# Performance work log

Hardware: AMD Instinct MI355X
Metric: run time of the kernel (lower is better)

The kernel has to match this reference:

```python
import jax, jax.numpy as jnp
import numpy as np

B, S, D = 2, 2048, 512
H = 8
G = 4
LAMBDA_INIT = 0.2  # 0.8 - 0.6*exp(-0.3*(layer_idx-1)) with layer_idx=1
EPS = 1e-5


def setup_inputs() -> dict:
    key = jax.random.key(0)
    ks = jax.random.split(key, 16)
    n = jax.random.normal
    return {
        "x": n(ks[0], (B, S, D), jnp.float32),
        "K1_w": n(ks[1], (D, D), jnp.float32) * 0.02,
        "K1_b": n(ks[2], (D,), jnp.float32) * 0.02,
        "Q1_w": n(ks[3], (D, D), jnp.float32) * 0.02,
        "K2_w": n(ks[4], (D, D), jnp.float32) * 0.02,
        "K2_b": n(ks[5], (D,), jnp.float32) * 0.02,
        "Q2_w": n(ks[6], (D, D), jnp.float32) * 0.02,
        "V_w": n(ks[7], (D, D), jnp.float32) * 0.02,
        "lambda_q1": n(ks[8], (H, 1), jnp.float32),
        "lambda_k1": n(ks[9], (H, 1), jnp.float32),
        "lambda_q2": n(ks[10], (H, 1), jnp.float32),
        "lambda_k2": n(ks[11], (H, 1), jnp.float32),
        "gn_w": jnp.ones((D,), jnp.float32),
        "gn_b": jnp.zeros((D,), jnp.float32),
        "out_w": n(ks[12], (D, D), jnp.float32) * 0.02,
        "out_b": n(ks[13], (D,), jnp.float32) * 0.02,
    }


def reference(x, K1_w, K1_b, Q1_w, K2_w, K2_b, Q2_w, V_w,
              lambda_q1, lambda_k1, lambda_q2, lambda_k2,
              gn_w, gn_b, out_w, out_b):
    b, s, d = x.shape
    hd = d // H

    def heads(t):  # (b,s,d) -> (b,H,s,hd)
        return t.reshape(b, s, H, hd).transpose(0, 2, 1, 3)

    q1 = heads(x @ Q1_w.T)
    k1 = heads(x @ K1_w.T + K1_b)
    q2 = heads(x @ Q2_w.T)
    k2 = heads(x @ K2_w.T + K2_b)
    v = heads(x @ V_w.T)

    scale = hd ** 0.5
    a1 = jax.nn.softmax(jnp.einsum('bhqd,bhkd->bhqk', q1, k1) / scale, axis=-1)
    a2 = jax.nn.softmax(jnp.einsum('bhqd,bhkd->bhqk', q2, k2) / scale, axis=-1)

    lam = (jnp.exp(lambda_q1 * lambda_k1)
           - jnp.exp(lambda_q2 * lambda_k2) + LAMBDA_INIT)  # (H,1)
    attn = a1 - lam.reshape(1, H, 1, 1) * a2

    o = jnp.einsum('bhqk,bhkd->bhqd', attn, v)
    o = o.transpose(0, 2, 1, 3).reshape(b, s, d)

    # GroupNorm over channels: input (b, d, s), groups G normalize over (d/G, s)
    xc = o.transpose(0, 2, 1).reshape(b, G, d // G, s)
    mu = xc.mean(axis=(2, 3), keepdims=True)
    var = xc.var(axis=(2, 3), keepdims=True)
    xn = ((xc - mu) * jax.lax.rsqrt(var + EPS)).reshape(b, d, s)
    xn = xn * gn_w[None, :, None] + gn_b[None, :, None]

    y = xn.transpose(0, 2, 1) @ out_w.T + out_b
    return y
```

## Files before the change

kernel.cpp:

```cpp
#include <hip/hip_runtime.h>
#include <hip/hip_bf16.h>

typedef __bf16 bf16;
typedef __attribute__((ext_vector_type(8))) __bf16 bf16x8;
typedef __attribute__((ext_vector_type(4))) float f32x4;

#define MFMA16(a, b, c) __builtin_amdgcn_mfma_f32_16x16x32_bf16((a), (b), (c), 0, 0, 0)

static constexpr float EPS = 1e-5f;
static constexpr float LAMBDA_INIT = 0.2f;
static constexpr float LOG2E = 1.44269504088896340736f;

__device__ __forceinline__ bf16x8 cvt8(const float* p) {
    const f32x4 a = *(const f32x4*)p;
    const f32x4 b = *(const f32x4*)(p + 4);
    bf16x8 r;
    r[0] = (bf16)a[0]; r[1] = (bf16)a[1]; r[2] = (bf16)a[2]; r[3] = (bf16)a[3];
    r[4] = (bf16)b[0]; r[5] = (bf16)b[1]; r[6] = (bf16)b[2]; r[7] = (bf16)b[3];
    return r;
}

__device__ __forceinline__ void gload_lds16(const void* g, void* l) {
    __builtin_amdgcn_global_load_lds(
        (const __attribute__((address_space(1))) unsigned int*)g,
        (__attribute__((address_space(3))) unsigned int*)l,
        16, 0, 0);
}

__global__ __launch_bounds__(256) void prep_kernel(
    const float* __restrict__ x,
    const float* __restrict__ q1w, const float* __restrict__ k1w,
    const float* __restrict__ q2w, const float* __restrict__ k2w,
    const float* __restrict__ vw,
    const float* __restrict__ ow, const float* __restrict__ gnw,
    const float* __restrict__ gnb,
    bf16* __restrict__ xb, bf16* __restrict__ wb,
    bf16* __restrict__ owg, float* __restrict__ S0, float* __restrict__ stats)
{
    const int tid = threadIdx.x;
    if (blockIdx.x < 1664) {
        const size_t base = ((size_t)blockIdx.x * 256 + tid) * 8;
        if (base < 2097152) {
            *(bf16x8*)(xb + base) = cvt8(x + base);
        } else {
            const size_t wbase = base - 2097152;
            const int wsel = (int)(wbase >> 18);
            const size_t off = wbase & 262143;
            const float* W = (wsel == 0) ? q1w : (wsel == 1) ? k1w :
                             (wsel == 2) ? q2w : (wsel == 3) ? k2w : vw;
            *(bf16x8*)(wb + wbase) = cvt8(W + off);
        }
        return;
    }

    __shared__ float red[4];
    const int pb = blockIdx.x - 1664;
    if (pb == 0 && tid < 16) stats[tid] = 0.f;

    const int n0 = pb * 16;
    const int c0 = tid, c1 = tid + 256;
    const float gw0 = gnw[c0], gw1 = gnw[c1];
    const float gb0 = gnb[c0], gb1 = gnb[c1];

    for (int n = 0; n < 16; ++n) {
        const size_t rowb = (size_t)(n0 + n) * 512;
        const float w0 = ow[rowb + c0];
        const float w1 = ow[rowb + c1];
        owg[rowb + c0] = (bf16)(w0 * gw0);
        owg[rowb + c1] = (bf16)(w1 * gw1);
        float s = gb0 * w0 + gb1 * w1;
#pragma unroll
        for (int off = 1; off < 64; off <<= 1) s += __shfl_xor(s, off, 64);
        if ((tid & 63) == 0) red[tid >> 6] = s;
        __syncthreads();
        if (tid == 0) S0[n0 + n] = red[0] + red[1] + red[2] + red[3];
        __syncthreads();
    }
}

__global__ __launch_bounds__(256) void proj_kernel(
    const bf16* __restrict__ xb, const bf16* __restrict__ wb,
    const float* __restrict__ k1b, const float* __restrict__ k2b,
    bf16* __restrict__ q1o, bf16* __restrict__ k1o,
    bf16* __restrict__ q2o, bf16* __restrict__ k2o,
    bf16* __restrict__ vto)
{
    __shared__ __align__(16) bf16 As[2][128 * 32];
    __shared__ __align__(16) bf16 Bs[2][128 * 32];

    const int tid = threadIdx.x;
    const int wave = tid >> 6, lane = tid & 63;
    const int l15 = lane & 15, quad = lane >> 4;
    const int wm = wave >> 1, wn = wave & 1;

    const int mb = blockIdx.x / 20;
    const int nb = blockIdx.x % 20;
    const int wsel = nb >> 2;
    const int nrow0 = (nb & 3) * 128;

    const int srow = lane >> 2;
    const int scol = (lane & 3) * 8;
    const bf16* ag = xb + (size_t)(mb * 128 + srow) * 512 + scol;
    const bf16* bg = wb + (size_t)(wsel * 512 + nrow0 + srow) * 512 + scol;

    f32x4 acc[4][4];
#pragma unroll
    for (int i = 0; i < 4; ++i)
#pragma unroll
        for (int j = 0; j < 4; ++j)
            acc[i][j] = (f32x4){0.f, 0.f, 0.f, 0.f};

#pragma unroll
    for (int c = 0; c < 2; ++c) {
        const int chunk = wave * 2 + c;
        gload_lds16(ag + (size_t)(chunk * 16) * 512, As[0] + chunk * 512);
        gload_lds16(bg + (size_t)(chunk * 16) * 512, Bs[0] + chunk * 512);
    }
    __syncthreads();

    for (int s = 0; s < 16; ++s) {
        const int cur = s & 1;
        if (s < 15) {
            const int k0n = (s + 1) * 32;
#pragma unroll
            for (int c = 0; c < 2; ++c) {
                const int chunk = wave * 2 + c;
                gload_lds16(ag + (size_t)(chunk * 16) * 512 + k0n, As[cur ^ 1] + chunk * 512);
                gload_lds16(bg + (size_t)(chunk * 16) * 512 + k0n, Bs[cur ^ 1] + chunk * 512);
            }
        }

        const bf16* Ac = As[cur];
        const bf16* Bc = Bs[cur];
        bf16x8 af[4], bfr[4];
#pragma unroll
        for (int i = 0; i < 4; ++i)
            af[i] = *(const bf16x8*)(Ac + (wm * 64 + i * 16 + l15) * 32 + quad * 8);
#pragma unroll
        for (int j = 0; j < 4; ++j)
            bfr[j] = *(const bf16x8*)(Bc + (wn * 64 + j * 16 + l15) * 32 + quad * 8);

#pragma unroll
        for (int i = 0; i < 4; ++i)
#pragma unroll
            for (int j = 0; j < 4; ++j)
                acc[i][j] = MFMA16(af[i], bfr[j], acc[i][j]);

        __syncthreads();
    }

    const float scale = (wsel == 0 || wsel == 2) ? 0.125f * LOG2E : 1.0f;
#pragma unroll
    for (int j = 0; j < 4; ++j) {
        const int ncol = nrow0 + wn * 64 + j * 16 + l15;
        float bias = 0.f;
        if (wsel == 1) bias = k1b[ncol];
        if (wsel == 3) bias = k2b[ncol];
        const int h = ncol >> 6, hd = ncol & 63;
        const int xh = (hd >> 1) & 3;
#pragma unroll
        for (int i = 0; i < 4; ++i) {
#pragma unroll
            for (int r = 0; r < 4; ++r) {
                const int m = mb * 128 + wm * 64 + i * 16 + quad * 4 + r;
                const int bidx = m >> 11, s = m & 2047;
                const float v = acc[i][j][r] * scale + bias;
                if (wsel == 4) {
                    const int s5 = s & 31;
                    const int q = (s5 >> 2) & 3;
                    const int jj = (s5 & 3) + ((s5 >> 4) << 2);
                    const int p = ((q ^ xh) << 3) | jj;
                    const int sp = (s & ~31) | p;
                    vto[((size_t)(bidx * 8 + h) * 64 + hd) * 2048 + sp] = (bf16)v;
                } else {
                    bf16* dst = (wsel == 0) ? q1o : (wsel == 1) ? k1o :
                                (wsel == 2) ? q2o : k2o;
                    dst[((size_t)(bidx * 8 + h) * 2048 + s) * 64 + hd] = (bf16)v;
                }
            }
        }
    }
}

__global__ __launch_bounds__(512, 4) void attn_kernel(
    const bf16* __restrict__ q1, const bf16* __restrict__ k1,
    const bf16* __restrict__ q2, const bf16* __restrict__ k2,
    const bf16* __restrict__ vt,
    const float* __restrict__ lq1, const float* __restrict__ lk1,
    const float* __restrict__ lq2, const float* __restrict__ lk2,
    bf16* __restrict__ o, float* __restrict__ stats)
{
    __shared__ __align__(16) bf16 smem[2][12288];
    __shared__ float lbuf[8][2][16];
    __shared__ float sred[8][2];

    const int tid = threadIdx.x;
    const int wave = tid >> 6;
    const int lane = tid & 63;
    const int l15 = lane & 15, quad = lane >> 4;
    const int qtile = wave & 3;
    const int kg = wave >> 2;

    const int rid = (blockIdx.x & 7) * 64 + (blockIdx.x >> 3);
    const int bh = rid >> 5;
    const int qt = rid & 31;
    const int b = bh >> 3, h = bh & 7;

    const bf16* k1t = k1 + (size_t)bh * 2048 * 64;
    const bf16* k2t = k2 + (size_t)bh * 2048 * 64;
    const bf16* vtt = vt + (size_t)bh * 64 * 2048;

    const int qrow = qt * 64 + qtile * 16 + l15;
    const bf16* q1p = q1 + ((size_t)bh * 2048 + qrow) * 64 + quad * 8;
    const bf16* q2p = q2 + ((size_t)bh * 2048 + qrow) * 64 + quad * 8;
    const bf16x8 q1f0 = *(const bf16x8*)(q1p);
    const bf16x8 q1f1 = *(const bf16x8*)(q1p + 32);
    const bf16x8 q2f0 = *(const bf16x8*)(q2p);
    const bf16x8 q2f1 = *(const bf16x8*)(q2p + 32);

    const int sw = wave & 3;
    const int skey0 = (wave < 4) ? 0 : 1024;
    const size_t ksrc0 = (size_t)(skey0 + sw * 8 + (lane >> 3)) * 64
                       + 8 * ((lane & 7) ^ (lane >> 3));
    const size_t vsrc0 = (size_t)(sw * 16 + (lane >> 2)) * 2048 + skey0 + (lane & 3) * 8;

    const int koffa = 8 * (quad ^ (l15 & 7));
    const int koffb = 8 * ((quad + 4) ^ (l15 & 7));
    const int vsw = 8 * (quad ^ ((l15 >> 1) & 3));

    f32x4 O1[4], O2[4];
    float l1 = 0.f, l2 = 0.f;
#pragma unroll
    for (int t = 0; t < 4; ++t) {
        O1[t] = (f32x4){0.f, 0.f, 0.f, 0.f};
        O2[t] = (f32x4){0.f, 0.f, 0.f, 0.f};
    }

    gload_lds16(k1t + ksrc0, smem[0] + wave * 512);
    gload_lds16(k2t + ksrc0, smem[0] + 4096 + wave * 512);
    gload_lds16(vtt + vsrc0, smem[0] + 8192 + wave * 512);
    __syncthreads();

    for (int it = 0; it < 32; ++it) {
        const int cur = it & 1;
        const bf16* sb = smem[cur];

        if (it < 31) {
            bf16* nb_ = smem[cur ^ 1];
            const size_t koff = ksrc0 + (size_t)(it + 1) * 32 * 64;
            gload_lds16(k1t + koff, nb_ + wave * 512);
            gload_lds16(k2t + koff, nb_ + 4096 + wave * 512);
            gload_lds16(vtt + vsrc0 + (it + 1) * 32, nb_ + 8192 + wave * 512);
        }

        const bf16* k1r = sb + kg * 2048;
        const bf16* k2r = sb + 4096 + kg * 2048;
        const bf16* vr  = sb + 8192 + kg * 2048;

        const bf16x8 k1t0a = *(const bf16x8*)(k1r + l15 * 64 + koffa);
        const bf16x8 k1t0b = *(const bf16x8*)(k1r + l15 * 64 + koffb);
        const bf16x8 k1t1a = *(const bf16x8*)(k1r + (16 + l15) * 64 + koffa);
        const bf16x8 k1t1b = *(const bf16x8*)(k1r + (16 + l15) * 64 + koffb);
        const bf16x8 k2t0a = *(const bf16x8*)(k2r + l15 * 64 + koffa);
        const bf16x8 k2t0b = *(const bf16x8*)(k2r + l15 * 64 + koffb);
        const bf16x8 k2t1a = *(const bf16x8*)(k2r + (16 + l15) * 64 + koffa);
        const bf16x8 k2t1b = *(const bf16x8*)(k2r + (16 + l15) * 64 + koffb);
        const bf16x8 v0 = *(const bf16x8*)(vr + l15 * 32 + vsw);
        const bf16x8 v1 = *(const bf16x8*)(vr + (16 + l15) * 32 + vsw);
        const bf16x8 v2 = *(const bf16x8*)(vr + (32 + l15) * 32 + vsw);
        const bf16x8 v3 = *(const bf16x8*)(vr + (48 + l15) * 32 + vsw);

        f32x4 z = (f32x4){0.f, 0.f, 0.f, 0.f};
        f32x4 s1t0 = MFMA16(k1t0a, q1f0, z);  s1t0 = MFMA16(k1t0b, q1f1, s1t0);
        f32x4 s1t1 = MFMA16(k1t1a, q1f0, z);  s1t1 = MFMA16(k1t1b, q1f1, s1t1);
        f32x4 s2t0 = MFMA16(k2t0a, q2f0, z);  s2t0 = MFMA16(k2t0b, q2f1, s2t0);
        f32x4 s2t1 = MFMA16(k2t1a, q2f0, z);  s2t1 = MFMA16(k2t1b, q2f1, s2t1);

        bf16x8 b1, b2;
#pragma unroll
        for (int r = 0; r < 4; ++r) {
            float e;
            e = __builtin_amdgcn_exp2f(s1t0[r]); l1 += e; b1[r]     = (bf16)e;
            e = __builtin_amdgcn_exp2f(s1t1[r]); l1 += e; b1[4 + r] = (bf16)e;
            e = __builtin_amdgcn_exp2f(s2t0[r]); l2 += e; b2[r]     = (bf16)e;
            e = __builtin_amdgcn_exp2f(s2t1[r]); l2 += e; b2[4 + r] = (bf16)e;
        }

        O1[0] = MFMA16(v0, b1, O1[0]);
        O1[1] = MFMA16(v1, b1, O1[1]);
        O1[2] = MFMA16(v2, b1, O1[2]);
        O1[3] = MFMA16(v3, b1, O1[3]);
        O2[0] = MFMA16(v0, b2, O2[0]);
        O2[1] = MFMA16(v1, b2, O2[1]);
        O2[2] = MFMA16(v2, b2, O2[2]);
        O2[3] = MFMA16(v3, b2, O2[3]);

        __syncthreads();
    }

    l1 += __shfl_xor(l1, 16, 64);  l1 += __shfl_xor(l1, 32, 64);
    l2 += __shfl_xor(l2, 16, 64);  l2 += __shfl_xor(l2, 32, 64);
    if (lane < 16) {
        lbuf[wave][0][lane] = l1;
        lbuf[wave][1][lane] = l2;
    }
    __syncthreads();

    f32x4* rb = (f32x4*)smem;
    if (wave == 4 || wave == 5) {
        f32x4* dst = rb + (wave - 4) * 512;
#pragma unroll
        for (int t = 0; t < 4; ++t) {
            dst[t * 64 + lane]       = O1[t];
            dst[(4 + t) * 64 + lane] = O2[t];
        }
    }
    __syncthreads();
    if (wave == 0 || wave == 1) {
        const f32x4* src = rb + wave * 512;
#pragma unroll
        for (int t = 0; t < 4; ++t) {
            O1[t] += src[t * 64 + lane];
            O2[t] += src[(4 + t) * 64 + lane];
        }
    }
    __syncthreads();
    if (wave == 6 || wave == 7) {
        f32x4* dst = rb + (wave - 6) * 512;
#pragma unroll
        for (int t = 0; t < 4; ++t) {
            dst[t * 64 + lane]       = O1[t];
            dst[(4 + t) * 64 + lane] = O2[t];
        }
    }
    __syncthreads();
    if (wave == 2 || wave == 3) {
        const f32x4* src = rb + (wave - 2) * 512;
#pragma unroll
        for (int t = 0; t < 4; ++t) {
            O1[t] += src[t * 64 + lane];
            O2[t] += src[(4 + t) * 64 + lane];
        }
    }

    float ssum = 0.f, ssq = 0.f;
    if (wave < 4) {
        const float L1 = l1 + lbuf[wave + 4][0][l15];
        const float L2 = l2 + lbuf[wave + 4][1][l15];
        const float lam = __expf(lq1[h] * lk1[h]) - __expf(lq2[h] * lk2[h]) + LAMBDA_INIT;
        const float inv1 = 1.f / L1;
        const float inv2 = lam / L2;
        const size_t row = (size_t)(b * 2048 + qt * 64 + wave * 16 + l15) * 512 + h * 64;
#pragma unroll
        for (int t = 0; t < 4; ++t) {
#pragma unroll
            for (int r = 0; r < 4; ++r) {
                const float val = O1[t][r] * inv1 - O2[t][r] * inv2;
                ssum += val;
                ssq += val * val;
                o[row + t * 16 + quad * 4 + r] = (bf16)val;
            }
        }
    }
#pragma unroll
    for (int off = 1; off < 64; off <<= 1) {
        ssum += __shfl_xor(ssum, off, 64);
        ssq += __shfl_xor(ssq, off, 64);
    }
    if (lane == 0) { sred[wave][0] = ssum; sred[wave][1] = ssq; }
    __syncthreads();
    if (tid == 0) {
        float s0 = 0.f, s1 = 0.f;
        for (int w = 0; w < 8; ++w) { s0 += sred[w][0]; s1 += sred[w][1]; }
        const int bg = b * 4 + (h >> 1);
        atomicAdd(&stats[bg * 2], s0);
        atomicAdd(&stats[bg * 2 + 1], s1);
    }
}

__global__ __launch_bounds__(256) void out_gemm_kernel(
    const bf16* __restrict__ o, const bf16* __restrict__ owg,
    const float* __restrict__ S0, const float* __restrict__ stats,
    const float* __restrict__ ob, float* __restrict__ y)
{
    __shared__ __align__(16) bf16 As[2][64 * 32];
    __shared__ __align__(16) bf16 Bs[2][64 * 32];

    const int tid = threadIdx.x;
    const int wave = tid >> 6, lane = tid & 63;
    const int l15 = lane & 15, quad = lane >> 4;

    const int mb = blockIdx.x >> 3;
    const int nb = blockIdx.x & 7;
    const int b = mb >> 5;

    const float N = 128.f * 2048.f;
    float mu[4], rs[4];
#pragma unroll
    for (int g = 0; g < 4; ++g) {
        const float m = stats[(b * 4 + g) * 2] / N;
        const float var = stats[(b * 4 + g) * 2 + 1] / N - m * m;
        mu[g] = m;
        rs[g] = rsqrtf(var + EPS);
    }

    const int srow = wave * 16 + (lane >> 2);
    const int scol = (lane & 3) * 8;
    const bf16* ag = o + (size_t)(mb * 64 + srow) * 512 + scol;
    const bf16* bg = owg + (size_t)(nb * 64 + srow) * 512 + scol;

    f32x4 acc[4], tot[4];
#pragma unroll
    for (int i = 0; i < 4; ++i) {
        acc[i] = (f32x4){0.f, 0.f, 0.f, 0.f};
        tot[i] = (f32x4){0.f, 0.f, 0.f, 0.f};
    }
    float s1g[4];
    float s1p = 0.f;
#pragma unroll
    for (int g = 0; g < 4; ++g) s1g[g] = 0.f;

    gload_lds16(ag, As[0] + wave * 512);
    gload_lds16(bg, Bs[0] + wave * 512);
    __syncthreads();

    for (int kk = 0; kk < 16; ++kk) {
        const int cur = kk & 1;
        if (kk < 15) {
            gload_lds16(ag + (kk + 1) * 32, As[cur ^ 1] + wave * 512);
            gload_lds16(bg + (kk + 1) * 32, Bs[cur ^ 1] + wave * 512);
        }

        bf16x8 af[4];
#pragma unroll
        for (int i = 0; i < 4; ++i)
            af[i] = *(const bf16x8*)(As[cur] + (i * 16 + l15) * 32 + quad * 8);
        const bf16x8 bf = *(const bf16x8*)(Bs[cur] + (wave * 16 + l15) * 32 + quad * 8);

#pragma unroll
        for (int i = 0; i < 4; ++i)
            acc[i] = MFMA16(af[i], bf, acc[i]);

#pragma unroll
        for (int j = 0; j < 8; ++j) s1p += (float)bf[j];

        __syncthreads();

        if ((kk & 3) == 3) {
            const int g = kk >> 2;
#pragma unroll
            for (int i = 0; i < 4; ++i) {
#pragma unroll
                for (int r = 0; r < 4; ++r) tot[i][r] += rs[g] * acc[i][r];
                acc[i] = (f32x4){0.f, 0.f, 0.f, 0.f};
            }
            float sg = s1p + __shfl_xor(s1p, 16, 64);
            sg += __shfl_xor(sg, 32, 64);
            s1g[g] = sg;
            s1p = 0.f;
        }
    }

    const int ncol = nb * 64 + wave * 16 + l15;
    float bias = S0[ncol] + ob[ncol];
#pragma unroll
    for (int g = 0; g < 4; ++g) bias -= mu[g] * rs[g] * s1g[g];

#pragma unroll
    for (int i = 0; i < 4; ++i) {
#pragma unroll
        for (int r = 0; r < 4; ++r) {
            const int m = mb * 64 + i * 16 + quad * 4 + r;
            y[(size_t)m * 512 + ncol] = tot[i][r] + bias;
        }
    }
}

extern "C" void kernel_launch(void* const* d_in, const int* in_sizes, int n_in,
                              void* d_out, int out_size, void* d_ws, size_t ws_size,
                              hipStream_t stream)
{
    const float* x   = (const float*)d_in[0];
    const float* K1w = (const float*)d_in[1];
    const float* K1b = (const float*)d_in[2];
    const float* Q1w = (const float*)d_in[3];
    const float* K2w = (const float*)d_in[4];
    const float* K2b = (const float*)d_in[5];
    const float* Q2w = (const float*)d_in[6];
    const float* Vw  = (const float*)d_in[7];
    const float* lq1 = (const float*)d_in[8];
    const float* lk1 = (const float*)d_in[9];
    const float* lq2 = (const float*)d_in[10];
    const float* lk2 = (const float*)d_in[11];
    const float* gnw = (const float*)d_in[12];
    const float* gnb = (const float*)d_in[13];
    const float* Ow  = (const float*)d_in[14];
    const float* Ob  = (const float*)d_in[15];

    const size_t SZ = (size_t)2 * 8 * 2048 * 64;
    bf16* q1 = (bf16*)d_ws;
    bf16* k1 = q1 + SZ;
    bf16* q2 = k1 + SZ;
    bf16* k2 = q2 + SZ;
    bf16* vt = k2 + SZ;
    bf16* o  = vt + SZ;
    bf16* xb = o;
    bf16* wb = o + SZ;
    bf16* owg = wb + (size_t)2560 * 512;
    float* S0 = (float*)(owg + 512 * 512);
    float* stats = S0 + 512;

    prep_kernel<<<1696, 256, 0, stream>>>(x, Q1w, K1w, Q2w, K2w, Vw,
                                          Ow, gnw, gnb, xb, wb, owg, S0, stats);
    proj_kernel<<<640, 256, 0, stream>>>(xb, wb, K1b, K2b,
                                         q1, k1, q2, k2, vt);
    attn_kernel<<<512, 512, 0, stream>>>(q1, k1, q2, k2, vt,
                                         lq1, lk1, lq2, lk2, o, stats);
    out_gemm_kernel<<<512, 256, 0, stream>>>(o, owg, S0, stats, Ob,
                                             (float*)d_out);
}
```

Baseline: 181.7 us.

## Widen GEMM K-tiles to 64 with swizzled LDS and halve attention waves

The projection and output GEMMs now stage K-tiles of 64 instead of 32 through an XOR-swizzled LDS layout. This halves the number of barrier-separated iterations and is meant to cut bank conflicts. The attention kernel drops from 8 to 4 waves per block, with each wave handling two 16-row query tiles so every K/V fragment read from LDS is reused twice. It also adds s_setprio around the MFMA bursts and simplifies the cross-wave reduction. In exchange, register pressure rises and fewer waves are resident to hide latency.

```diff
diff --git a/kernel.cpp b/kernel.cpp
--- a/kernel.cpp
+++ b/kernel.cpp
@@ -85,8 +85,8 @@
     bf16* __restrict__ q2o, bf16* __restrict__ k2o,
     bf16* __restrict__ vto)
 {
-    __shared__ __align__(16) bf16 As[2][128 * 32];
-    __shared__ __align__(16) bf16 Bs[2][128 * 32];
+    __shared__ __align__(16) bf16 As[2][128 * 64];
+    __shared__ __align__(16) bf16 Bs[2][128 * 64];
 
     const int tid = threadIdx.x;
     const int wave = tid >> 6, lane = tid & 63;
@@ -98,8 +98,8 @@
     const int wsel = nb >> 2;
     const int nrow0 = (nb & 3) * 128;
 
-    const int srow = lane >> 2;
-    const int scol = (lane & 3) * 8;
+    const int srow = lane >> 3;
+    const int scol = 8 * ((lane & 7) ^ srow);
     const bf16* ag = xb + (size_t)(mb * 128 + srow) * 512 + scol;
     const bf16* bg = wb + (size_t)(wsel * 512 + nrow0 + srow) * 512 + scol;
 
@@ -110,41 +110,48 @@
         for (int j = 0; j < 4; ++j)
             acc[i][j] = (f32x4){0.f, 0.f, 0.f, 0.f};
 
-#pragma unroll
-    for (int c = 0; c < 2; ++c) {
-        const int chunk = wave * 2 + c;
-        gload_lds16(ag + (size_t)(chunk * 16) * 512, As[0] + chunk * 512);
-        gload_lds16(bg + (size_t)(chunk * 16) * 512, Bs[0] + chunk * 512);
-    }
+#define STAGE_PROJ(buf, s) do {                                                \
+    const int k0_ = (s) * 64;                                                  \
+    _Pragma("unroll")                                                          \
+    for (int c_ = 0; c_ < 4; ++c_) {                                           \
+        const int chunk_ = wave * 4 + c_;                                      \
+        gload_lds16(ag + (size_t)(chunk_ * 8) * 512 + k0_, As[buf] + chunk_ * 512); \
+        gload_lds16(bg + (size_t)(chunk_ * 8) * 512 + k0_, Bs[buf] + chunk_ * 512); \
+    }                                                                          \
+} while (0)
+
+    STAGE_PROJ(0, 0);
     __syncthreads();
 
-    for (int s = 0; s < 16; ++s) {
+    const int ka = 8 * (quad ^ (l15 & 7));
+
+    for (int s = 0; s < 8; ++s) {
         const int cur = s & 1;
-        if (s < 15) {
-            const int k0n = (s + 1) * 32;
-#pragma unroll
-            for (int c = 0; c < 2; ++c) {
-                const int chunk = wave * 2 + c;
-                gload_lds16(ag + (size_t)(chunk * 16) * 512 + k0n, As[cur ^ 1] + chunk * 512);
-                gload_lds16(bg + (size_t)(chunk * 16) * 512 + k0n, Bs[cur ^ 1] + chunk * 512);
-            }
-        }
+        if (s < 7) STAGE_PROJ(cur ^ 1, s + 1);
 
         const bf16* Ac = As[cur];
         const bf16* Bc = Bs[cur];
-        bf16x8 af[4], bfr[4];
+        bf16x8 al[4], ah[4], bl[4], bh_[4];
+#pragma unroll
+        for (int i = 0; i < 4; ++i) {
+            const bf16* p = Ac + (wm * 64 + i * 16 + l15) * 64;
+            al[i] = *(const bf16x8*)(p + ka);
+            ah[i] = *(const bf16x8*)(p + (ka ^ 32));
+        }
+#pragma unroll
+        for (int j = 0; j < 4; ++j) {
+            const bf16* p = Bc + (wn * 64 + j * 16 + l15) * 64;
+            bl[j]  = *(const bf16x8*)(p + ka);
+            bh_[j] = *(const bf16x8*)(p + (ka ^ 32));
+        }
+
 #pragma unroll
         for (int i = 0; i < 4; ++i)
-            af[i] = *(const bf16x8*)(Ac + (wm * 64 + i * 16 + l15) * 32 + quad * 8);
-#pragma unroll
-        for (int j = 0; j < 4; ++j)
-            bfr[j] = *(const bf16x8*)(Bc + (wn * 64 + j * 16 + l15) * 32 + quad * 8);
-
-#pragma unroll
-        for (int i = 0; i < 4; ++i)
-#pragma unroll
-            for (int j = 0; j < 4; ++j)
-                acc[i][j] = MFMA16(af[i], bfr[j], acc[i][j]);
+#pragma unroll
+            for (int j = 0; j < 4; ++j) {
+                acc[i][j] = MFMA16(al[i], bl[j], acc[i][j]);
+                acc[i][j] = MFMA16(ah[i], bh_[j], acc[i][j]);
+            }
 
         __syncthreads();
     }
@@ -182,7 +189,7 @@
     }
 }
 
-__global__ __launch_bounds__(512, 4) void attn_kernel(
+__global__ __launch_bounds__(256, 2) void attn_kernel(
     const bf16* __restrict__ q1, const bf16* __restrict__ k1,
     const bf16* __restrict__ q2, const bf16* __restrict__ k2,
     const bf16* __restrict__ vt,
@@ -191,15 +198,15 @@
     bf16* __restrict__ o, float* __restrict__ stats)
 {
     __shared__ __align__(16) bf16 smem[2][12288];
-    __shared__ float lbuf[8][2][16];
-    __shared__ float sred[8][2];
+    __shared__ float lbuf[4][4][16];
+    __shared__ float sred[2][2];
 
     const int tid = threadIdx.x;
     const int wave = tid >> 6;
     const int lane = tid & 63;
     const int l15 = lane & 15, quad = lane >> 4;
-    const int qtile = wave & 3;
-    const int kg = wave >> 2;
+    const int qp = wave & 1;
+    const int kg = wave >> 1;
 
     const int rid = (blockIdx.x & 7) * 64 + (blockIdx.x >> 3);
     const int bh = rid >> 5;
@@ -210,48 +217,57 @@
     const bf16* k2t = k2 + (size_t)bh * 2048 * 64;
     const bf16* vtt = vt + (size_t)bh * 64 * 2048;
 
-    const int qrow = qt * 64 + qtile * 16 + l15;
+    const int qrow = qt * 64 + qp * 32 + l15;
     const bf16* q1p = q1 + ((size_t)bh * 2048 + qrow) * 64 + quad * 8;
     const bf16* q2p = q2 + ((size_t)bh * 2048 + qrow) * 64 + quad * 8;
-    const bf16x8 q1f0 = *(const bf16x8*)(q1p);
-    const bf16x8 q1f1 = *(const bf16x8*)(q1p + 32);
-    const bf16x8 q2f0 = *(const bf16x8*)(q2p);
-    const bf16x8 q2f1 = *(const bf16x8*)(q2p + 32);
-
-    const int sw = wave & 3;
-    const int skey0 = (wave < 4) ? 0 : 1024;
-    const size_t ksrc0 = (size_t)(skey0 + sw * 8 + (lane >> 3)) * 64
-                       + 8 * ((lane & 7) ^ (lane >> 3));
-    const size_t vsrc0 = (size_t)(sw * 16 + (lane >> 2)) * 2048 + skey0 + (lane & 3) * 8;
+    const bf16x8 q1A0 = *(const bf16x8*)(q1p);
+    const bf16x8 q1A1 = *(const bf16x8*)(q1p + 32);
+    const bf16x8 q1B0 = *(const bf16x8*)(q1p + 16 * 64);
+    const bf16x8 q1B1 = *(const bf16x8*)(q1p + 16 * 64 + 32);
+    const bf16x8 q2A0 = *(const bf16x8*)(q2p);
+    const bf16x8 q2A1 = *(const bf16x8*)(q2p + 32);
+    const bf16x8 q2B0 = *(const bf16x8*)(q2p + 16 * 64);
+    const bf16x8 q2B1 = *(const bf16x8*)(q2p + 16 * 64 + 32);
+
+    const int krow = lane >> 3;
+    const int kcol = 8 * ((lane & 7) ^ krow);
+    const int ko0 = (wave * 8 + krow) * 64 + kcol;
+    const int ko1 = (1024 + wave * 8 + krow) * 64 + kcol;
+    const int vrow = lane >> 2;
+    const int vo0 = (wave * 16 + vrow) * 2048 + (lane & 3) * 8;
+    const int vo1 = (wave * 16 + vrow) * 2048 + 1024 + (lane & 3) * 8;
+
+#define STAGE_ATTN(buf, itv) do {                                   \
+    const int ko_ = (itv) * 32 * 64;                                \
+    const int vo_ = (itv) * 32;                                     \
+    gload_lds16(k1t + ko0 + ko_, (buf) + wave * 512);               \
+    gload_lds16(k1t + ko1 + ko_, (buf) + 2048 + wave * 512);        \
+    gload_lds16(k2t + ko0 + ko_, (buf) + 4096 + wave * 512);        \
+    gload_lds16(k2t + ko1 + ko_, (buf) + 6144 + wave * 512);        \
+    gload_lds16(vtt + vo0 + vo_, (buf) + 8192 + wave * 512);        \
+    gload_lds16(vtt + vo1 + vo_, (buf) + 10240 + wave * 512);       \
+} while (0)
 
     const int koffa = 8 * (quad ^ (l15 & 7));
     const int koffb = 8 * ((quad + 4) ^ (l15 & 7));
     const int vsw = 8 * (quad ^ ((l15 >> 1) & 3));
 
-    f32x4 O1[4], O2[4];
-    float l1 = 0.f, l2 = 0.f;
+    f32x4 O1A[4], O2A[4], O1B[4], O2B[4];
+    float l1A = 0.f, l2A = 0.f, l1B = 0.f, l2B = 0.f;
 #pragma unroll
     for (int t = 0; t < 4; ++t) {
-        O1[t] = (f32x4){0.f, 0.f, 0.f, 0.f};
-        O2[t] = (f32x4){0.f, 0.f, 0.f, 0.f};
-    }
-
-    gload_lds16(k1t + ksrc0, smem[0] + wave * 512);
-    gload_lds16(k2t + ksrc0, smem[0] + 4096 + wave * 512);
-    gload_lds16(vtt + vsrc0, smem[0] + 8192 + wave * 512);
+        O1A[t] = (f32x4){0.f, 0.f, 0.f, 0.f};
+        O2A[t] = (f32x4){0.f, 0.f, 0.f, 0.f};
+        O1B[t] = (f32x4){0.f, 0.f, 0.f, 0.f};
+        O2B[t] = (f32x4){0.f, 0.f, 0.f, 0.f};
+    }
+
+    STAGE_ATTN(smem[0], 0);
     __syncthreads();
 
     for (int it = 0; it < 32; ++it) {
-        const int cur = it & 1;
-        const bf16* sb = smem[cur];
-
-        if (it < 31) {
-            bf16* nb_ = smem[cur ^ 1];
-            const size_t koff = ksrc0 + (size_t)(it + 1) * 32 * 64;
-            gload_lds16(k1t + koff, nb_ + wave * 512);
-            gload_lds16(k2t + koff, nb_ + 4096 + wave * 512);
-            gload_lds16(vtt + vsrc0 + (it + 1) * 32, nb_ + 8192 + wave * 512);
-        }
+        const bf16* sb = smem[it & 1];
+        if (it < 31) STAGE_ATTN(smem[(it & 1) ^ 1], it + 1);
 
         const bf16* k1r = sb + kg * 2048;
         const bf16* k2r = sb + 4096 + kg * 2048;
@@ -270,95 +286,99 @@
         const bf16x8 v2 = *(const bf16x8*)(vr + (32 + l15) * 32 + vsw);
         const bf16x8 v3 = *(const bf16x8*)(vr + (48 + l15) * 32 + vsw);
 
-        f32x4 z = (f32x4){0.f, 0.f, 0.f, 0.f};
-        f32x4 s1t0 = MFMA16(k1t0a, q1f0, z);  s1t0 = MFMA16(k1t0b, q1f1, s1t0);
-        f32x4 s1t1 = MFMA16(k1t1a, q1f0, z);  s1t1 = MFMA16(k1t1b, q1f1, s1t1);
-        f32x4 s2t0 = MFMA16(k2t0a, q2f0, z);  s2t0 = MFMA16(k2t0b, q2f1, s2t0);
-        f32x4 s2t1 = MFMA16(k2t1a, q2f0, z);  s2t1 = MFMA16(k2t1b, q2f1, s2t1);
-
-        bf16x8 b1, b2;
+        const f32x4 z = (f32x4){0.f, 0.f, 0.f, 0.f};
+        __builtin_amdgcn_s_setprio(1);
+        f32x4 s1t0A = MFMA16(k1t0a, q1A0, z);  s1t0A = MFMA16(k1t0b, q1A1, s1t0A);
+        f32x4 s1t1A = MFMA16(k1t1a, q1A0, z);  s1t1A = MFMA16(k1t1b, q1A1, s1t1A);
+        f32x4 s2t0A = MFMA16(k2t0a, q2A0, z);  s2t0A = MFMA16(k2t0b, q2A1, s2t0A);
+        f32x4 s2t1A = MFMA16(k2t1a, q2A0, z);  s2t1A = MFMA16(k2t1b, q2A1, s2t1A);
+        f32x4 s1t0B = MFMA16(k1t0a, q1B0, z);  s1t0B = MFMA16(k1t0b, q1B1, s1t0B);
+        f32x4 s1t1B = MFMA16(k1t1a, q1B0, z);  s1t1B = MFMA16(k1t1b, q1B1, s1t1B);
+        f32x4 s2t0B = MFMA16(k2t0a, q2B0, z);  s2t0B = MFMA16(k2t0b, q2B1, s2t0B);
+        f32x4 s2t1B = MFMA16(k2t1a, q2B0, z);  s2t1B = MFMA16(k2t1b, q2B1, s2t1B);
+        __builtin_amdgcn_s_setprio(0);
+
+        bf16x8 b1A, b2A, b1B, b2B;
 #pragma unroll
         for (int r = 0; r < 4; ++r) {
             float e;
-            e = __builtin_amdgcn_exp2f(s1t0[r]); l1 += e; b1[r]     = (bf16)e;
-            e = __builtin_amdgcn_exp2f(s1t1[r]); l1 += e; b1[4 + r] = (bf16)e;
-            e = __builtin_amdgcn_exp2f(s2t0[r]); l2 += e; b2[r]     = (bf16)e;
-            e = __builtin_amdgcn_exp2f(s2t1[r]); l2 += e; b2[4 + r] = (bf16)e;
-        }
-
-        O1[0] = MFMA16(v0, b1, O1[0]);
-        O1[1] = MFMA16(v1, b1, O1[1]);
-        O1[2] = MFMA16(v2, b1, O1[2]);
-        O1[3] = MFMA16(v3, b1, O1[3]);
-        O2[0] = MFMA16(v0, b2, O2[0]);
-        O2[1] = MFMA16(v1, b2, O2[1]);
-        O2[2] = MFMA16(v2, b2, O2[2]);
-        O2[3] = MFMA16(v3, b2, O2[3]);
+            e = __builtin_amdgcn_exp2f(s1t0A[r]); l1A += e; b1A[r]     = (bf16)e;
+            e = __builtin_amdgcn_exp2f(s1t1A[r]); l1A += e; b1A[4 + r] = (bf16)e;
+            e = __builtin_amdgcn_exp2f(s2t0A[r]); l2A += e; b2A[r]     = (bf16)e;
+            e = __builtin_amdgcn_exp2f(s2t1A[r]); l2A += e; b2A[4 + r] = (bf16)e;
+            e = __builtin_amdgcn_exp2f(s1t0B[r]); l1B += e; b1B[r]     = (bf16)e;
+            e = __builtin_amdgcn_exp2f(s1t1B[r]); l1B += e; b1B[4 + r] = (bf16)e;
+            e = __builtin_amdgcn_exp2f(s2t0B[r]); l2B += e; b2B[r]     = (bf16)e;
+            e = __builtin_amdgcn_exp2f(s2t1B[r]); l2B += e; b2B[4 + r] = (bf16)e;
+        }
+
+        __builtin_amdgcn_s_setprio(1);
+        O1A[0] = MFMA16(v0, b1A, O1A[0]);  O1A[1] = MFMA16(v1, b1A, O1A[1]);
+        O1A[2] = MFMA16(v2, b1A, O1A[2]);  O1A[3] = MFMA16(v3, b1A, O1A[3]);
+        O2A[0] = MFMA16(v0, b2A, O2A[0]);  O2A[1] = MFMA16(v1, b2A, O2A[1]);
+        O2A[2] = MFMA16(v2, b2A, O2A[2]);  O2A[3] = MFMA16(v3, b2A, O2A[3]);
+        O1B[0] = MFMA16(v0, b1B, O1B[0]);  O1B[1] = MFMA16(v1, b1B, O1B[1]);
+        O1B[2] = MFMA16(v2, b1B, O1B[2]);  O1B[3] = MFMA16(v3, b1B, O1B[3]);
+        O2B[0] = MFMA16(v0, b2B, O2B[0]);  O2B[1] = MFMA16(v1, b2B, O2B[1]);
+        O2B[2] = MFMA16(v2, b2B, O2B[2]);  O2B[3] = MFMA16(v3, b2B, O2B[3]);
+        __builtin_amdgcn_s_setprio(0);
 
         __syncthreads();
     }
 
-    l1 += __shfl_xor(l1, 16, 64);  l1 += __shfl_xor(l1, 32, 64);
-    l2 += __shfl_xor(l2, 16, 64);  l2 += __shfl_xor(l2, 32, 64);
+    l1A += __shfl_xor(l1A, 16, 64);  l1A += __shfl_xor(l1A, 32, 64);
+    l2A += __shfl_xor(l2A, 16, 64);  l2A += __shfl_xor(l2A, 32, 64);
+    l1B += __shfl_xor(l1B, 16, 64);  l1B += __shfl_xor(l1B, 32, 64);
+    l2B += __shfl_xor(l2B, 16, 64);  l2B += __shfl_xor(l2B, 32, 64);
     if (lane < 16) {
-        lbuf[wave][0][lane] = l1;
-        lbuf[wave][1][lane] = l2;
+        lbuf[wave][0][lane] = l1A;
+        lbuf[wave][1][lane] = l2A;
+        lbuf[wave][2][lane] = l1B;
+        lbuf[wave][3][lane] = l2B;
+    }
+
+    f32x4* rb = (f32x4*)smem;
+    if (kg == 1) {
+        f32x4* dst = rb + qp * 1024;
+#pragma unroll
+        for (int t = 0; t < 4; ++t) {
+            dst[t * 64 + lane]        = O1A[t];
+            dst[(4 + t) * 64 + lane]  = O2A[t];
+            dst[(8 + t) * 64 + lane]  = O1B[t];
+            dst[(12 + t) * 64 + lane] = O2B[t];
+        }
     }
     __syncthreads();
 
-    f32x4* rb = (f32x4*)smem;
-    if (wave == 4 || wave == 5) {
-        f32x4* dst = rb + (wave - 4) * 512;
+    float ssum = 0.f, ssq = 0.f;
+    if (kg == 0) {
+        const f32x4* src = rb + qp * 1024;
 #pragma unroll
         for (int t = 0; t < 4; ++t) {
-            dst[t * 64 + lane]       = O1[t];
-            dst[(4 + t) * 64 + lane] = O2[t];
-        }
-    }
-    __syncthreads();
-    if (wave == 0 || wave == 1) {
-        const f32x4* src = rb + wave * 512;
+            O1A[t] += src[t * 64 + lane];
+            O2A[t] += src[(4 + t) * 64 + lane];
+            O1B[t] += src[(8 + t) * 64 + lane];
+            O2B[t] += src[(12 + t) * 64 + lane];
+        }
+        const float L1A = l1A + lbuf[wave + 2][0][l15];
+        const float L2A = l2A + lbuf[wave + 2][1][l15];
+        const float L1B = l1B + lbuf[wave + 2][2][l15];
+        const float L2B = l2B + lbuf[wave + 2][3][l15];
+        const float lam = __expf(lq1[h] * lk1[h]) - __expf(lq2[h] * lk2[h]) + LAMBDA_INIT;
+        const float i1A = 1.f / L1A, i2A = lam / L2A;
+        const float i1B = 1.f / L1B, i2B = lam / L2B;
+        const size_t rowA = (size_t)(b * 2048 + qt * 64 + qp * 32 + l15) * 512 + h * 64;
+        const size_t rowB = rowA + 16 * 512;
 #pragma unroll
         for (int t = 0; t < 4; ++t) {
-            O1[t] += src[t * 64 + lane];
-            O2[t] += src[(4 + t) * 64 + lane];
-        }
-    }
-    __syncthreads();
-    if (wave == 6 || wave == 7) {
-        f32x4* dst = rb + (wave - 6) * 512;
-#pragma unroll
-        for (int t = 0; t < 4; ++t) {
-            dst[t * 64 + lane]       = O1[t];
-            dst[(4 + t) * 64 + lane] = O2[t];
-        }
-    }
-    __syncthreads();
-    if (wave == 2 || wave == 3) {
-        const f32x4* src = rb + (wave - 2) * 512;
-#pragma unroll
-        for (int t = 0; t < 4; ++t) {
-            O1[t] += src[t * 64 + lane];
-            O2[t] += src[(4 + t) * 64 + lane];
-        }
-    }
-
-    float ssum = 0.f, ssq = 0.f;
-    if (wave < 4) {
-        const float L1 = l1 + lbuf[wave + 4][0][l15];
-        const float L2 = l2 + lbuf[wave + 4][1][l15];
-        const float lam = __expf(lq1[h] * lk1[h]) - __expf(lq2[h] * lk2[h]) + LAMBDA_INIT;
-        const float inv1 = 1.f / L1;
-        const float inv2 = lam / L2;
-        const size_t row = (size_t)(b * 2048 + qt * 64 + wave * 16 + l15) * 512 + h * 64;
-#pragma unroll
-        for (int t = 0; t < 4; ++t) {
 #pragma unroll
             for (int r = 0; r < 4; ++r) {
-                const float val = O1[t][r] * inv1 - O2[t][r] * inv2;
-                ssum += val;
-                ssq += val * val;
-                o[row + t * 16 + quad * 4 + r] = (bf16)val;
+                const float vA = O1A[t][r] * i1A - O2A[t][r] * i2A;
+                const float vB = O1B[t][r] * i1B - O2B[t][r] * i2B;
+                ssum += vA + vB;
+                ssq += vA * vA + vB * vB;
+                o[rowA + t * 16 + quad * 4 + r] = (bf16)vA;
+                o[rowB + t * 16 + quad * 4 + r] = (bf16)vB;
             }
         }
     }
@@ -367,11 +387,11 @@
         ssum += __shfl_xor(ssum, off, 64);
         ssq += __shfl_xor(ssq, off, 64);
     }
-    if (lane == 0) { sred[wave][0] = ssum; sred[wave][1] = ssq; }
+    if (kg == 0 && lane == 0) { sred[qp][0] = ssum; sred[qp][1] = ssq; }
     __syncthreads();
     if (tid == 0) {
-        float s0 = 0.f, s1 = 0.f;
-        for (int w = 0; w < 8; ++w) { s0 += sred[w][0]; s1 += sred[w][1]; }
+        const float s0 = sred[0][0] + sred[1][0];
+        const float s1 = sred[0][1] + sred[1][1];
         const int bg = b * 4 + (h >> 1);
         atomicAdd(&stats[bg * 2], s0);
         atomicAdd(&stats[bg * 2 + 1], s1);
@@ -383,8 +403,8 @@
     const float* __restrict__ S0, const float* __restrict__ stats,
     const float* __restrict__ ob, float* __restrict__ y)
 {
-    __shared__ __align__(16) bf16 As[2][64 * 32];
-    __shared__ __align__(16) bf16 Bs[2][64 * 32];
+    __shared__ __align__(16) bf16 As[2][64 * 64];
+    __shared__ __align__(16) bf16 Bs[2][64 * 64];
 
     const int tid = threadIdx.x;
     const int wave = tid >> 6, lane = tid & 63;
@@ -404,10 +424,20 @@
         rs[g] = rsqrtf(var + EPS);
     }
 
-    const int srow = wave * 16 + (lane >> 2);
-    const int scol = (lane & 3) * 8;
+    const int srow = lane >> 3;
+    const int scol = 8 * ((lane & 7) ^ srow);
     const bf16* ag = o + (size_t)(mb * 64 + srow) * 512 + scol;
     const bf16* bg = owg + (size_t)(nb * 64 + srow) * 512 + scol;
+
+#define STAGE_OUT(buf, s) do {                                                 \
+    const int k0_ = (s) * 64;                                                  \
+    _Pragma("unroll")                                                          \
+    for (int c_ = 0; c_ < 2; ++c_) {                                           \
+        const int chunk_ = wave * 2 + c_;                                      \
+        gload_lds16(ag + (size_t)(chunk_ * 8) * 512 + k0_, As[buf] + chunk_ * 512); \
+        gload_lds16(bg + (size_t)(chunk_ * 8) * 512 + k0_, Bs[buf] + chunk_ * 512); \
+    }                                                                          \
+} while (0)
 
     f32x4 acc[4], tot[4];
 #pragma unroll
@@ -420,34 +450,39 @@
 #pragma unroll
     for (int g = 0; g < 4; ++g) s1g[g] = 0.f;
 
-    gload_lds16(ag, As[0] + wave * 512);
-    gload_lds16(bg, Bs[0] + wave * 512);
+    STAGE_OUT(0, 0);
     __syncthreads();
 
-    for (int kk = 0; kk < 16; ++kk) {
+    const int ka = 8 * (quad ^ (l15 & 7));
+
+    for (int kk = 0; kk < 8; ++kk) {
         const int cur = kk & 1;
-        if (kk < 15) {
-            gload_lds16(ag + (kk + 1) * 32, As[cur ^ 1] + wave * 512);
-            gload_lds16(bg + (kk + 1) * 32, Bs[cur ^ 1] + wave * 512);
-        }
-
-        bf16x8 af[4];
-#pragma unroll
-        for (int i = 0; i < 4; ++i)
-            af[i] = *(const bf16x8*)(As[cur] + (i * 16 + l15) * 32 + quad * 8);
-        const bf16x8 bf = *(const bf16x8*)(Bs[cur] + (wave * 16 + l15) * 32 + quad * 8);
-
-#pragma unroll
-        for (int i = 0; i < 4; ++i)
-            acc[i] = MFMA16(af[i], bf, acc[i]);
-
-#pragma unroll
-        for (int j = 0; j < 8; ++j) s1p += (float)bf[j];
+        if (kk < 7) STAGE_OUT(cur ^ 1, kk + 1);
+
+        bf16x8 al[4], ah[4];
+#pragma unroll
+        for (int i = 0; i < 4; ++i) {
+            const bf16* p = As[cur] + (i * 16 + l15) * 64;
+            al[i] = *(const bf16x8*)(p + ka);
+            ah[i] = *(const bf16x8*)(p + (ka ^ 32));
+        }
+        const bf16* pb = Bs[cur] + (wave * 16 + l15) * 64;
+        const bf16x8 bl = *(const bf16x8*)(pb + ka);
+        const bf16x8 bh = *(const bf16x8*)(pb + (ka ^ 32));
+
+#pragma unroll
+        for (int i = 0; i < 4; ++i) {
+            acc[i] = MFMA16(al[i], bl, acc[i]);
+            acc[i] = MFMA16(ah[i], bh, acc[i]);
+        }
+
+#pragma unroll
+        for (int j = 0; j < 8; ++j) s1p += (float)bl[j] + (float)bh[j];
 
         __syncthreads();
 
-        if ((kk & 3) == 3) {
-            const int g = kk >> 2;
+        if (kk & 1) {
+            const int g = kk >> 1;
 #pragma unroll
             for (int i = 0; i < 4; ++i) {
 #pragma unroll
@@ -514,7 +549,7 @@
                                           Ow, gnw, gnb, xb, wb, owg, S0, stats);
     proj_kernel<<<640, 256, 0, stream>>>(xb, wb, K1b, K2b,
                                          q1, k1, q2, k2, vt);
-    attn_kernel<<<512, 512, 0, stream>>>(q1, k1, q2, k2, vt,
+    attn_kernel<<<512, 256, 0, stream>>>(q1, k1, q2, k2, vt,
                                          lq1, lk1, lq2, lk2, o, stats);
     out_gemm_kernel<<<512, 256, 0, stream>>>(o, owg, S0, stats, Ob,
                                              (float*)d_out);
```

After: 185.1 us. About the same (+1.9%).
